# Kernel tuning notes

Hardware: AMD Instinct MI355X
Metric: run time of the kernel (lower is better)

Reference implementation:

```python
import jax, jax.numpy as jnp
import numpy as np

KH = KW = 3  # deform conv kernel
EPS = 1e-12  # F.normalize eps


def _deform_sample(img, u, v):
    """Flow-guided deformable sampling: bilinear gather of img at each of the
    9 kernel offsets shifted by the per-pixel flow (u=dx, v=dy).
    img: [B,C,H,W]; u,v: [B,1,H,W] -> returns [B,C,9,H,W]."""
    B, C, H, W = img.shape
    ky, kx = jnp.meshgrid(jnp.arange(KH) - 1, jnp.arange(KW) - 1, indexing='ij')
    ky = ky.reshape(1, 9, 1, 1).astype(img.dtype)
    kx = kx.reshape(1, 9, 1, 1).astype(img.dtype)
    iy = jnp.arange(H, dtype=img.dtype).reshape(1, 1, H, 1)
    ix = jnp.arange(W, dtype=img.dtype).reshape(1, 1, 1, W)
    py = iy + ky + v  # [B,9,H,W]
    px = ix + kx + u
    y0 = jnp.floor(py); x0 = jnp.floor(px)
    wy = py - y0; wx = px - x0  # bilinear weights
    y0i = y0.astype(jnp.int32); x0i = x0.astype(jnp.int32)
    flat = img.reshape(B, C, H * W)

    def gather(yi, xi):
        valid = ((yi >= 0) & (yi < H) & (xi >= 0) & (xi < W)).astype(img.dtype)
        idx = jnp.clip(yi, 0, H - 1) * W + jnp.clip(xi, 0, W - 1)  # [B,9,H,W]
        g = jax.vmap(lambda f, i: jnp.take(f, i.reshape(-1), axis=1))(flat, idx)
        return g.reshape(B, C, 9, H, W) * valid[:, None]

    s = (gather(y0i, x0i) * ((1 - wy) * (1 - wx))[:, None]
         + gather(y0i, x0i + 1) * ((1 - wy) * wx)[:, None]
         + gather(y0i + 1, x0i) * (wy * (1 - wx))[:, None]
         + gather(y0i + 1, x0i + 1) * (wy * wx)[:, None])
    return s


def setup_inputs() -> dict:
    key = jax.random.key(0)
    k1, k2, k3, k4, k5 = jax.random.split(key, 5)
    B, C, H, W = 2, 64, 256, 256
    num_heads = 4
    clone = jax.random.normal(k1, (B, C, H, W), dtype=jnp.float32)
    x = jax.random.normal(k2, (B, C, H * W), dtype=jnp.float32)
    u = jax.random.normal(k3, (B, 1, H, W), dtype=jnp.float32)
    v = jax.random.normal(k4, (B, 1, H, W), dtype=jnp.float32)
    weight = jax.random.normal(k5, (C, C, KH, KW), dtype=jnp.float32) * 0.05
    temperature = jnp.ones((num_heads, 1, 1), dtype=jnp.float32)
    return {"clone": clone, "x": x, "u": u, "v": v,
            "weight": weight, "temperature": temperature}


def reference(clone, x, u, v, weight, temperature):
    # deformable conv: bilinear gather then contract over (in_ch, kernel)
    s = _deform_sample(clone, u, v)                      # [B,C,9,H,W]
    w = weight.reshape(weight.shape[0], weight.shape[1], 9)
    conv = jnp.einsum('bckhw,ock->bohw', s, w)           # [B,C,H,W]
    B, C, H, W = conv.shape
    head = temperature.shape[0]
    kv = conv.reshape(B, head, C // head, H * W)          # k = v = deform output
    q = x.reshape(B, head, C // head, H * W)
    qn = q / jnp.maximum(jnp.linalg.norm(q, axis=-1, keepdims=True), EPS)
    kn = kv / jnp.maximum(jnp.linalg.norm(kv, axis=-1, keepdims=True), EPS)
    attn = jnp.einsum('bhcs,bhds->bhcd', qn, kn) * temperature  # [B,h,c,c]
    attn = jax.nn.softmax(attn, axis=-1)
    out = jnp.einsum('bhcd,bhds->bhcs', attn, kv)
    return out.reshape(B, C, H * W)
```

## Files before the change

### kernel.cpp

```cpp
#include <hip/hip_runtime.h>

typedef __bf16 bf16;
typedef __bf16 bf16x4 __attribute__((ext_vector_type(4)));
typedef __bf16 bf16x8 __attribute__((ext_vector_type(8)));
typedef float  f32x4  __attribute__((ext_vector_type(4)));

#define HH 256
#define WW 256
#define NB 2
#define NC 64
#define NS 65536
#define EX 258
#define NHEAD 4
#define DH 16

#define OFF_CLONET 0ul
#define OFF_CEXT   16777216ul
#define OFF_KV     33817600ul
#define OFF_WPK    50594816ul
#define OFF_ACC    50668544ul

__global__ __launch_bounds__(256) void k0t(const float* __restrict__ clone,
                                           bf16* __restrict__ cloneT,
                                           const float* __restrict__ wgt,
                                           bf16* __restrict__ wpk,
                                           float* __restrict__ accums) {
    const int xc = blockIdx.x;
    const int y  = blockIdx.y;
    const int b  = blockIdx.z;
    const int t  = threadIdx.x;

    if (b == 0 && y < 7) {
        int t2 = (y * 4 + xc) * 256 + t;
        if (t2 < 9 * 2 * 4 * 64) {
            int L   = t2 & 63;
            int mtg = (t2 >> 6) & 3;
            int kc  = (t2 >> 8) & 1;
            int tap = t2 >> 9;
            int o  = mtg * 16 + (L & 15);
            int cb = kc * 32 + (L >> 4) * 8;
            bf16x8 vv;
            #pragma unroll
            for (int j = 0; j < 8; j++)
                vv[j] = (bf16)wgt[(o * 64 + (cb + j)) * 9 + tap];
            *(bf16x8*)(wpk + t2 * 8) = vv;
        }
        int z = t2 - 9 * 2 * 4 * 64;
        if (z >= 0 && z < 2304) accums[z] = 0.0f;
    }

    __shared__ bf16 sm[64 * 68];
    {
        const int c = t >> 2, q = t & 3;
        const float* src = clone + ((size_t)(b * NC + c) * HH + y) * WW + xc * 64 + q * 16;
        #pragma unroll
        for (int i = 0; i < 4; i++) {
            f32x4 f = *(const f32x4*)(src + i * 4);
            bf16x4 h;
            #pragma unroll
            for (int j = 0; j < 4; j++) h[j] = (bf16)f[j];
            *(bf16x4*)(sm + c * 68 + q * 16 + i * 4) = h;
        }
    }
    __syncthreads();
    {
        const int x = t >> 2, cq = t & 3;
        bf16x8 o0, o1;
        #pragma unroll
        for (int j = 0; j < 8; j++) {
            o0[j] = sm[(cq * 16 + j) * 68 + x];
            o1[j] = sm[(cq * 16 + 8 + j) * 68 + x];
        }
        bf16* dst = cloneT + (((size_t)(b * HH + y) * WW + xc * 64 + x) << 6) + cq * 16;
        *(bf16x8*)(dst)     = o0;
        *(bf16x8*)(dst + 8) = o1;
    }
}

__global__ __launch_bounds__(256, 2) void k1_conv(const bf16* __restrict__ cloneT,
                                                  const bf16* __restrict__ wpk,
                                                  bf16* __restrict__ cext) {
    const int Xt = blockIdx.x;
    const int Yt = blockIdx.y;
    const int b  = blockIdx.z;
    const int t  = threadIdx.x;
    const int L  = t & 63;
    const int wv = t >> 6;
    const int mpair = wv >> 1;
    const int npair = wv & 1;

    extern __shared__ bf16 tile[];

    bf16x8 afrag[2][9][2];
    #pragma unroll
    for (int mt = 0; mt < 2; mt++)
        #pragma unroll
        for (int tap = 0; tap < 9; tap++)
            #pragma unroll
            for (int kc = 0; kc < 2; kc++) {
                int idx = ((tap * 2 + kc) * 4 + (mpair * 2 + mt)) * 64 + L;
                afrag[mt][tap][kc] = *(const bf16x8*)(wpk + idx * 8);
            }

    for (int r = 0; r < 8; r++) {
        int y = Yt * 6 - 2 + r;
        bool yin = (y >= 0) && (y < HH);
        for (int j = t; j < 528; j += 256) {
            int col = j >> 3, ck = j & 7;
            int xg = Xt * 64 - 2 + col;
            bf16x8 val;
            if (yin && xg >= 0 && xg < WW) {
                val = *(const bf16x8*)(cloneT + (((size_t)(b * HH + y) * WW + xg) << 6) + ck * 8);
            } else {
                #pragma unroll
                for (int e = 0; e < 8; e++) val[e] = (bf16)0.0f;
            }
            *(bf16x8*)(tile + (r * 66 + col) * 72 + ck * 8) = val;
        }
    }
    __syncthreads();

    const f32x4 zero4 = {0.0f, 0.0f, 0.0f, 0.0f};
    for (int Yi = 0; Yi < 6; Yi++) {
        f32x4 acc[2][2];
        acc[0][0] = zero4; acc[0][1] = zero4; acc[1][0] = zero4; acc[1][1] = zero4;
        #pragma unroll
        for (int tap = 0; tap < 9; tap++) {
            const int ky = tap / 3 - 1;
            const int kx = tap % 3 - 1;
            const int r = Yi + 1 + ky;
            #pragma unroll
            for (int kc = 0; kc < 2; kc++) {
                const int cb = kc * 32 + (L >> 4) * 8;
                #pragma unroll
                for (int nt = 0; nt < 2; nt++) {
                    const int col = npair * 32 + nt * 16 + (L & 15) + kx + 1;
                    bf16x8 bfrag = *(const bf16x8*)(tile + (r * 66 + col) * 72 + cb);
                    #pragma unroll
                    for (int mt = 0; mt < 2; mt++)
                        acc[mt][nt] = __builtin_amdgcn_mfma_f32_16x16x32_bf16(
                            afrag[mt][tap][kc], bfrag, acc[mt][nt], 0, 0, 0);
                }
            }
        }
        int Yp = Yt * 6 + Yi;
        #pragma unroll
        for (int mt = 0; mt < 2; mt++)
            #pragma unroll
            for (int nt = 0; nt < 2; nt++) {
                int Xp = Xt * 64 + npair * 32 + nt * 16 + (L & 15);
                if (Xp < EX) {
                    int o = mpair * 32 + mt * 16 + (L >> 4) * 4;
                    bf16x4 st;
                    #pragma unroll
                    for (int rg = 0; rg < 4; rg++) st[rg] = (bf16)acc[mt][nt][rg];
                    *(bf16x4*)(cext + ((((size_t)b * EX + Yp) * EX + Xp) << 6) + o) = st;
                }
            }
    }
}

__global__ __launch_bounds__(256) void k2_gather(const float* __restrict__ uu,
                                                 const float* __restrict__ vv,
                                                 const bf16* __restrict__ cext,
                                                 bf16* __restrict__ kv) {
    int gid = blockIdx.x * 256 + threadIdx.x;
    int ckh = gid >> 17;
    int idx = gid & 131071;
    int b  = idx >> 16;
    int hw = idx & 65535;
    int hy = hw >> 8;
    int wx = hw & 255;
    float fv = vv[idx];
    float fu = uu[idx];
    float py = (float)hy + fv;
    float px = (float)wx + fu;
    float fy = floorf(py);
    float fx = floorf(px);
    float ay = py - fy;
    float ax = px - fx;
    int ys = (int)fy + 1;
    int xs = (int)fx + 1;
    float w00 = (1.0f - ay) * (1.0f - ax);
    float w01 = (1.0f - ay) * ax;
    float w10 = ay * (1.0f - ax);
    float w11 = ay * ax;
    bool y0i = (ys >= 0) && (ys < EX);
    bool y1i = (ys + 1 >= 0) && (ys + 1 < EX);
    bool x0i = (xs >= 0) && (xs < EX);
    bool x1i = (xs + 1 >= 0) && (xs + 1 < EX);
    if (!y0i) { w00 = 0.0f; w01 = 0.0f; }
    if (!y1i) { w10 = 0.0f; w11 = 0.0f; }
    if (!x0i) { w00 = 0.0f; w10 = 0.0f; }
    if (!x1i) { w01 = 0.0f; w11 = 0.0f; }
    int y0c = ys < 0 ? 0 : (ys > EX - 1 ? EX - 1 : ys);
    int y1c = ys + 1 < 0 ? 0 : (ys + 1 > EX - 1 ? EX - 1 : ys + 1);
    int x0c = xs < 0 ? 0 : (xs > EX - 1 ? EX - 1 : xs);
    int x1c = xs + 1 < 0 ? 0 : (xs + 1 > EX - 1 ? EX - 1 : xs + 1);
    const bf16* pb = cext + (((size_t)b * EX * EX) << 6);
    size_t i00 = ((size_t)(y0c * EX + x0c)) << 6;
    size_t i01 = ((size_t)(y0c * EX + x1c)) << 6;
    size_t i10 = ((size_t)(y1c * EX + x0c)) << 6;
    size_t i11 = ((size_t)(y1c * EX + x1c)) << 6;
    bf16* kvp = kv + (((size_t)(b * NC + ckh * 32)) << 16) + hw;
    #pragma unroll
    for (int ck = 0; ck < 4; ck++) {
        int c0 = ckh * 32 + ck * 8;
        bf16x8 c00 = *(const bf16x8*)(pb + i00 + c0);
        bf16x8 c01 = *(const bf16x8*)(pb + i01 + c0);
        bf16x8 c10 = *(const bf16x8*)(pb + i10 + c0);
        bf16x8 c11 = *(const bf16x8*)(pb + i11 + c0);
        #pragma unroll
        for (int j = 0; j < 8; j++) {
            float val = w00 * (float)c00[j] + w01 * (float)c01[j]
                      + w10 * (float)c10[j] + w11 * (float)c11[j];
            kvp[((size_t)(ck * 8 + j)) << 16] = (bf16)val;
        }
    }
}

__global__ __launch_bounds__(256) void k3_dots(const float* __restrict__ x,
                                               const bf16* __restrict__ kv,
                                               float* __restrict__ dots,
                                               float* __restrict__ qss,
                                               float* __restrict__ kss) {
    const int ch = blockIdx.x;
    const int h  = blockIdx.y;
    const int b  = blockIdx.z;
    const int t  = threadIdx.x;
    const int L  = t & 63;
    const int wv = t >> 6;
    const int row = L & 15;
    const int kg  = L >> 4;
    const float* qb = x + ((size_t)(b * NC + h * DH + row)) * NS;
    const bf16*  kb = kv + (((size_t)(b * NC + h * DH + row)) << 16);
    f32x4 acc = {0.0f, 0.0f, 0.0f, 0.0f};
    float qp = 0.0f, kp = 0.0f;
    const int s0 = ch * 1024 + wv * 256 + kg * 8;
    for (int it = 0; it < 8; it++) {
        int s = s0 + it * 32;
        f32x4 q0 = *(const f32x4*)(qb + s);
        f32x4 q1 = *(const f32x4*)(qb + s + 4);
        bf16x8 ka = *(const bf16x8*)(kb + s);
        bf16x8 qa;
        #pragma unroll
        for (int j = 0; j < 4; j++) {
            qa[j]     = (bf16)q0[j];
            qa[j + 4] = (bf16)q1[j];
        }
        qp += q0[0]*q0[0] + q0[1]*q0[1] + q0[2]*q0[2] + q0[3]*q0[3]
            + q1[0]*q1[0] + q1[1]*q1[1] + q1[2]*q1[2] + q1[3]*q1[3];
        #pragma unroll
        for (int j = 0; j < 8; j++) {
            float kf = (float)ka[j];
            kp += kf * kf;
        }
        acc = __builtin_amdgcn_mfma_f32_16x16x32_bf16(qa, ka, acc, 0, 0, 0);
    }
    __shared__ float ldsD[256];
    __shared__ float ldsQ[16];
    __shared__ float ldsK[16];
    ldsD[t] = 0.0f;
    if (t < 16) { ldsQ[t] = 0.0f; ldsK[t] = 0.0f; }
    __syncthreads();
    #pragma unroll
    for (int rg = 0; rg < 4; rg++)
        atomicAdd(&ldsD[(kg * 4 + rg) * 16 + row], acc[rg]);
    atomicAdd(&ldsQ[row], qp);
    atomicAdd(&ldsK[row], kp);
    __syncthreads();
    const int bh = b * NHEAD + h;
    atomicAdd(&dots[bh * 256 + t], ldsD[t]);
    if (t < 16) {
        atomicAdd(&qss[bh * 16 + t], ldsQ[t]);
        atomicAdd(&kss[bh * 16 + t], ldsK[t]);
    }
}

__global__ __launch_bounds__(256) void k5_out(const bf16* __restrict__ kv,
                                              const float* __restrict__ dots,
                                              const float* __restrict__ qss,
                                              const float* __restrict__ kss,
                                              const float* __restrict__ temp,
                                              float* __restrict__ out) {
    const int ci = blockIdx.x;
    const int h  = blockIdx.y;
    const int b  = blockIdx.z;
    const int t  = threadIdx.x;
    const int bh = b * NHEAD + h;
    __shared__ float l[256];
    __shared__ float a[256];
    {
        int i = t >> 4, j = t & 15;
        float qn = fmaxf(sqrtf(qss[bh * 16 + i]), 1e-12f);
        float kn = fmaxf(sqrtf(kss[bh * 16 + j]), 1e-12f);
        float logit = dots[bh * 256 + t] / (qn * kn) * temp[h];
        l[t] = logit;
        __syncthreads();
        float mx = -1e30f;
        #pragma unroll
        for (int jj = 0; jj < 16; jj++) mx = fmaxf(mx, l[i * 16 + jj]);
        float sum = 0.0f;
        #pragma unroll
        for (int jj = 0; jj < 16; jj++) sum += expf(l[i * 16 + jj] - mx);
        a[t] = expf(logit - mx) / sum;
        __syncthreads();
    }
    const int s = (ci * 256 + t) * 4;
    const bf16* kvb = kv + (((size_t)(b * NC + h * DH)) << 16) + s;
    f32x4 kf[16];
    #pragma unroll
    for (int j = 0; j < 16; j++) {
        bf16x4 kk = *(const bf16x4*)(kvb + ((size_t)j << 16));
        #pragma unroll
        for (int e = 0; e < 4; e++) kf[j][e] = (float)kk[e];
    }
    float* ob = out + ((size_t)(b * NC + h * DH)) * NS + s;
    #pragma unroll
    for (int i = 0; i < 16; i++) {
        f32x4 o = {0.0f, 0.0f, 0.0f, 0.0f};
        #pragma unroll
        for (int j = 0; j < 16; j++)
            o += a[i * 16 + j] * kf[j];
        *(f32x4*)(ob + (size_t)i * NS) = o;
    }
}

extern "C" void kernel_launch(void* const* d_in, const int* in_sizes, int n_in,
                              void* d_out, int out_size, void* d_ws, size_t ws_size,
                              hipStream_t stream) {
    const float* clone = (const float*)d_in[0];
    const float* x     = (const float*)d_in[1];
    const float* u     = (const float*)d_in[2];
    const float* v     = (const float*)d_in[3];
    const float* wgt   = (const float*)d_in[4];
    const float* temp  = (const float*)d_in[5];
    float* out = (float*)d_out;

    char* ws = (char*)d_ws;
    bf16*  cloneT = (bf16*) (ws + OFF_CLONET);
    bf16*  cext   = (bf16*) (ws + OFF_CEXT);
    bf16*  kv     = (bf16*) (ws + OFF_KV);
    bf16*  wpk    = (bf16*) (ws + OFF_WPK);
    float* accums = (float*)(ws + OFF_ACC);
    float* dots = accums;
    float* qss  = accums + 2048;
    float* kss  = accums + 2048 + 128;

    static bool attr_set = false;
    if (!attr_set) {
        hipFuncSetAttribute((const void*)k1_conv,
                            hipFuncAttributeMaxDynamicSharedMemorySize, 76032);
        attr_set = true;
    }

    k0t<<<dim3(4, 256, 2), 256, 0, stream>>>(clone, cloneT, wgt, wpk, accums);
    k1_conv<<<dim3(5, 43, 2), 256, 76032, stream>>>(cloneT, wpk, cext);
    k2_gather<<<1024, 256, 0, stream>>>(u, v, cext, kv);
    k3_dots<<<dim3(64, 4, 2), 256, 0, stream>>>(x, kv, dots, qss, kss);
    k5_out<<<dim3(64, 4, 2), 256, 0, stream>>>(kv, dots, qss, kss, temp, out);
}
```

Baseline: 184.7 us.

## Fuse clone transpose into conv tile load and merge gather with dots

Removes the separate transpose kernel. The conv kernel now reads fp32 clone directly, converting and transposing it into its LDS tile, which drops one full bf16 intermediate write and read. It also fuses the bilinear gather kernel with the q·k dot-product kernel, so each block gathers 256 pixels of kv and then reduces dots for all four heads on those pixels. The cost is a wider LDS tile, strided fp32 loads in the conv prologue, and global atomics from more blocks per head. The dots phase re-reads the kv values the same block just wrote, after a block barrier.

```diff
diff --git a/kernel.cpp b/kernel.cpp
--- a/kernel.cpp
+++ b/kernel.cpp
@@ -14,70 +14,32 @@
 #define NHEAD 4
 #define DH 16
 
-#define OFF_CLONET 0ul
-#define OFF_CEXT   16777216ul
-#define OFF_KV     33817600ul
-#define OFF_WPK    50594816ul
-#define OFF_ACC    50668544ul
-
-__global__ __launch_bounds__(256) void k0t(const float* __restrict__ clone,
-                                           bf16* __restrict__ cloneT,
-                                           const float* __restrict__ wgt,
-                                           bf16* __restrict__ wpk,
-                                           float* __restrict__ accums) {
-    const int xc = blockIdx.x;
-    const int y  = blockIdx.y;
-    const int b  = blockIdx.z;
-    const int t  = threadIdx.x;
-
-    if (b == 0 && y < 7) {
-        int t2 = (y * 4 + xc) * 256 + t;
-        if (t2 < 9 * 2 * 4 * 64) {
-            int L   = t2 & 63;
-            int mtg = (t2 >> 6) & 3;
-            int kc  = (t2 >> 8) & 1;
-            int tap = t2 >> 9;
-            int o  = mtg * 16 + (L & 15);
-            int cb = kc * 32 + (L >> 4) * 8;
-            bf16x8 vv;
-            #pragma unroll
-            for (int j = 0; j < 8; j++)
-                vv[j] = (bf16)wgt[(o * 64 + (cb + j)) * 9 + tap];
-            *(bf16x8*)(wpk + t2 * 8) = vv;
-        }
-        int z = t2 - 9 * 2 * 4 * 64;
-        if (z >= 0 && z < 2304) accums[z] = 0.0f;
-    }
-
-    __shared__ bf16 sm[64 * 68];
-    {
-        const int c = t >> 2, q = t & 3;
-        const float* src = clone + ((size_t)(b * NC + c) * HH + y) * WW + xc * 64 + q * 16;
-        #pragma unroll
-        for (int i = 0; i < 4; i++) {
-            f32x4 f = *(const f32x4*)(src + i * 4);
-            bf16x4 h;
-            #pragma unroll
-            for (int j = 0; j < 4; j++) h[j] = (bf16)f[j];
-            *(bf16x4*)(sm + c * 68 + q * 16 + i * 4) = h;
-        }
-    }
-    __syncthreads();
-    {
-        const int x = t >> 2, cq = t & 3;
-        bf16x8 o0, o1;
-        #pragma unroll
-        for (int j = 0; j < 8; j++) {
-            o0[j] = sm[(cq * 16 + j) * 68 + x];
-            o1[j] = sm[(cq * 16 + 8 + j) * 68 + x];
-        }
-        bf16* dst = cloneT + (((size_t)(b * HH + y) * WW + xc * 64 + x) << 6) + cq * 16;
-        *(bf16x8*)(dst)     = o0;
-        *(bf16x8*)(dst + 8) = o1;
-    }
-}
-
-__global__ __launch_bounds__(256, 2) void k1_conv(const bf16* __restrict__ cloneT,
+#define OFF_CEXT   0ul
+#define OFF_KV     17040384ul
+#define OFF_WPK    33817600ul
+#define OFF_ACC    33891328ul
+
+__global__ void k0w(const float* __restrict__ wgt, bf16* __restrict__ wpk,
+                    float* __restrict__ accums) {
+    int t = blockIdx.x * 256 + threadIdx.x;
+    if (t < 9 * 2 * 4 * 64) {
+        int L   = t & 63;
+        int mtg = (t >> 6) & 3;
+        int kc  = (t >> 8) & 1;
+        int tap = t >> 9;
+        int o  = mtg * 16 + (L & 15);
+        int cb = kc * 32 + (L >> 4) * 8;
+        bf16x8 vv;
+        #pragma unroll
+        for (int j = 0; j < 8; j++)
+            vv[j] = (bf16)wgt[(o * 64 + (cb + j)) * 9 + tap];
+        *(bf16x8*)(wpk + t * 8) = vv;
+    }
+    int z = t - 9 * 2 * 4 * 64;
+    if (z >= 0 && z < 2304) accums[z] = 0.0f;
+}
+
+__global__ __launch_bounds__(256, 2) void k1_conv(const float* __restrict__ clone,
                                                   const bf16* __restrict__ wpk,
                                                   bf16* __restrict__ cext) {
     const int Xt = blockIdx.x;
@@ -102,20 +64,36 @@
                 afrag[mt][tap][kc] = *(const bf16x8*)(wpk + idx * 8);
             }
 
-    for (int r = 0; r < 8; r++) {
-        int y = Yt * 6 - 2 + r;
+    for (int u = t; u < 2176; u += 256) {
+        int xq = u % 17;
+        int rc = u / 17;
+        int cg = rc & 15;
+        int r  = rc >> 4;
+        int y  = Yt * 6 - 2 + r;
+        int xg0 = Xt * 64 - 4 + xq * 4;
+        int c0 = cg * 4;
+        f32x4 f[4];
         bool yin = (y >= 0) && (y < HH);
-        for (int j = t; j < 528; j += 256) {
-            int col = j >> 3, ck = j & 7;
-            int xg = Xt * 64 - 2 + col;
-            bf16x8 val;
-            if (yin && xg >= 0 && xg < WW) {
-                val = *(const bf16x8*)(cloneT + (((size_t)(b * HH + y) * WW + xg) << 6) + ck * 8);
-            } else {
+        if (yin && xg0 >= 0 && xg0 + 3 < WW) {
+            #pragma unroll
+            for (int i = 0; i < 4; i++)
+                f[i] = *(const f32x4*)(clone + ((size_t)(b * NC + c0 + i) * HH + y) * WW + xg0);
+        } else {
+            #pragma unroll
+            for (int i = 0; i < 4; i++)
                 #pragma unroll
-                for (int e = 0; e < 8; e++) val[e] = (bf16)0.0f;
-            }
-            *(bf16x8*)(tile + (r * 66 + col) * 72 + ck * 8) = val;
+                for (int e = 0; e < 4; e++) {
+                    int xg = xg0 + e;
+                    f[i][e] = (yin && xg >= 0 && xg < WW)
+                            ? clone[((size_t)(b * NC + c0 + i) * HH + y) * WW + xg] : 0.0f;
+                }
+        }
+        #pragma unroll
+        for (int e = 0; e < 4; e++) {
+            bf16x4 h;
+            #pragma unroll
+            for (int i = 0; i < 4; i++) h[i] = (bf16)f[i][e];
+            *(bf16x4*)(tile + (r * 68 + xq * 4 + e) * 72 + c0) = h;
         }
     }
     __syncthreads();
@@ -134,8 +112,8 @@
                 const int cb = kc * 32 + (L >> 4) * 8;
                 #pragma unroll
                 for (int nt = 0; nt < 2; nt++) {
-                    const int col = npair * 32 + nt * 16 + (L & 15) + kx + 1;
-                    bf16x8 bfrag = *(const bf16x8*)(tile + (r * 66 + col) * 72 + cb);
+                    const int col = npair * 32 + nt * 16 + (L & 15) + kx + 3;
+                    bf16x8 bfrag = *(const bf16x8*)(tile + (r * 68 + col) * 72 + cb);
                     #pragma unroll
                     for (int mt = 0; mt < 2; mt++)
                         acc[mt][nt] = __builtin_amdgcn_mfma_f32_16x16x32_bf16(
@@ -160,85 +138,88 @@
     }
 }
 
-__global__ __launch_bounds__(256) void k2_gather(const float* __restrict__ uu,
-                                                 const float* __restrict__ vv,
-                                                 const bf16* __restrict__ cext,
-                                                 bf16* __restrict__ kv) {
-    int gid = blockIdx.x * 256 + threadIdx.x;
-    int ckh = gid >> 17;
-    int idx = gid & 131071;
-    int b  = idx >> 16;
-    int hw = idx & 65535;
-    int hy = hw >> 8;
-    int wx = hw & 255;
-    float fv = vv[idx];
-    float fu = uu[idx];
-    float py = (float)hy + fv;
-    float px = (float)wx + fu;
-    float fy = floorf(py);
-    float fx = floorf(px);
-    float ay = py - fy;
-    float ax = px - fx;
-    int ys = (int)fy + 1;
-    int xs = (int)fx + 1;
-    float w00 = (1.0f - ay) * (1.0f - ax);
-    float w01 = (1.0f - ay) * ax;
-    float w10 = ay * (1.0f - ax);
-    float w11 = ay * ax;
-    bool y0i = (ys >= 0) && (ys < EX);
-    bool y1i = (ys + 1 >= 0) && (ys + 1 < EX);
-    bool x0i = (xs >= 0) && (xs < EX);
-    bool x1i = (xs + 1 >= 0) && (xs + 1 < EX);
-    if (!y0i) { w00 = 0.0f; w01 = 0.0f; }
-    if (!y1i) { w10 = 0.0f; w11 = 0.0f; }
-    if (!x0i) { w00 = 0.0f; w10 = 0.0f; }
-    if (!x1i) { w01 = 0.0f; w11 = 0.0f; }
-    int y0c = ys < 0 ? 0 : (ys > EX - 1 ? EX - 1 : ys);
-    int y1c = ys + 1 < 0 ? 0 : (ys + 1 > EX - 1 ? EX - 1 : ys + 1);
-    int x0c = xs < 0 ? 0 : (xs > EX - 1 ? EX - 1 : xs);
-    int x1c = xs + 1 < 0 ? 0 : (xs + 1 > EX - 1 ? EX - 1 : xs + 1);
-    const bf16* pb = cext + (((size_t)b * EX * EX) << 6);
-    size_t i00 = ((size_t)(y0c * EX + x0c)) << 6;
-    size_t i01 = ((size_t)(y0c * EX + x1c)) << 6;
-    size_t i10 = ((size_t)(y1c * EX + x0c)) << 6;
-    size_t i11 = ((size_t)(y1c * EX + x1c)) << 6;
-    bf16* kvp = kv + (((size_t)(b * NC + ckh * 32)) << 16) + hw;
-    #pragma unroll
-    for (int ck = 0; ck < 4; ck++) {
-        int c0 = ckh * 32 + ck * 8;
-        bf16x8 c00 = *(const bf16x8*)(pb + i00 + c0);
-        bf16x8 c01 = *(const bf16x8*)(pb + i01 + c0);
-        bf16x8 c10 = *(const bf16x8*)(pb + i10 + c0);
-        bf16x8 c11 = *(const bf16x8*)(pb + i11 + c0);
-        #pragma unroll
-        for (int j = 0; j < 8; j++) {
-            float val = w00 * (float)c00[j] + w01 * (float)c01[j]
-                      + w10 * (float)c10[j] + w11 * (float)c11[j];
-            kvp[((size_t)(ck * 8 + j)) << 16] = (bf16)val;
-        }
-    }
-}
-
-__global__ __launch_bounds__(256) void k3_dots(const float* __restrict__ x,
-                                               const bf16* __restrict__ kv,
-                                               float* __restrict__ dots,
-                                               float* __restrict__ qss,
-                                               float* __restrict__ kss) {
-    const int ch = blockIdx.x;
-    const int h  = blockIdx.y;
-    const int b  = blockIdx.z;
+
+__global__ __launch_bounds__(256) void k23(const float* __restrict__ uu,
+                                           const float* __restrict__ vv,
+                                           const bf16* __restrict__ cext,
+                                           const float* __restrict__ x,
+                                           bf16* __restrict__ kv,
+                                           float* __restrict__ dots,
+                                           float* __restrict__ qss,
+                                           float* __restrict__ kss) {
+    const int ci = blockIdx.x;
+    const int b  = blockIdx.y;
     const int t  = threadIdx.x;
-    const int L  = t & 63;
-    const int wv = t >> 6;
+
+    #pragma unroll
+    for (int it2 = 0; it2 < 2; it2++) {
+        int unit = it2 * 256 + t;
+        int ckh = unit >> 8;
+        int pix = unit & 255;
+        int hw = ci * 256 + pix;
+        int idx = b * NS + hw;
+        int hy = hw >> 8;
+        int wx = hw & 255;
+        float fv = vv[idx];
+        float fu = uu[idx];
+        float py = (float)hy + fv;
+        float px = (float)wx + fu;
+        float fy = floorf(py);
+        float fx = floorf(px);
+        float ay = py - fy;
+        float ax = px - fx;
+        int ys = (int)fy + 1;
+        int xs = (int)fx + 1;
+        float w00 = (1.0f - ay) * (1.0f - ax);
+        float w01 = (1.0f - ay) * ax;
+        float w10 = ay * (1.0f - ax);
+        float w11 = ay * ax;
+        bool y0i = (ys >= 0) && (ys < EX);
+        bool y1i = (ys + 1 >= 0) && (ys + 1 < EX);
+        bool x0i = (xs >= 0) && (xs < EX);
+        bool x1i = (xs + 1 >= 0) && (xs + 1 < EX);
+        if (!y0i) { w00 = 0.0f; w01 = 0.0f; }
+        if (!y1i) { w10 = 0.0f; w11 = 0.0f; }
+        if (!x0i) { w00 = 0.0f; w10 = 0.0f; }
+        if (!x1i) { w01 = 0.0f; w11 = 0.0f; }
+        int y0c = ys < 0 ? 0 : (ys > EX - 1 ? EX - 1 : ys);
+        int y1c = ys + 1 < 0 ? 0 : (ys + 1 > EX - 1 ? EX - 1 : ys + 1);
+        int x0c = xs < 0 ? 0 : (xs > EX - 1 ? EX - 1 : xs);
+        int x1c = xs + 1 < 0 ? 0 : (xs + 1 > EX - 1 ? EX - 1 : xs + 1);
+        const bf16* pb = cext + (((size_t)b * EX * EX) << 6);
+        size_t i00 = ((size_t)(y0c * EX + x0c)) << 6;
+        size_t i01 = ((size_t)(y0c * EX + x1c)) << 6;
+        size_t i10 = ((size_t)(y1c * EX + x0c)) << 6;
+        size_t i11 = ((size_t)(y1c * EX + x1c)) << 6;
+        bf16* kvp = kv + (((size_t)(b * NC + ckh * 32)) << 16) + hw;
+        #pragma unroll
+        for (int ck = 0; ck < 4; ck++) {
+            int c0 = ckh * 32 + ck * 8;
+            bf16x8 c00 = *(const bf16x8*)(pb + i00 + c0);
+            bf16x8 c01 = *(const bf16x8*)(pb + i01 + c0);
+            bf16x8 c10 = *(const bf16x8*)(pb + i10 + c0);
+            bf16x8 c11 = *(const bf16x8*)(pb + i11 + c0);
+            #pragma unroll
+            for (int j = 0; j < 8; j++) {
+                float val = w00 * (float)c00[j] + w01 * (float)c01[j]
+                          + w10 * (float)c10[j] + w11 * (float)c11[j];
+                kvp[((size_t)(ck * 8 + j)) << 16] = (bf16)val;
+            }
+        }
+    }
+    __syncthreads();
+
+    const int L = t & 63;
+    const int w = t >> 6;
     const int row = L & 15;
     const int kg  = L >> 4;
-    const float* qb = x + ((size_t)(b * NC + h * DH + row)) * NS;
-    const bf16*  kb = kv + (((size_t)(b * NC + h * DH + row)) << 16);
+    const float* qb = x  + ((size_t)(b * NC + w * DH + row)) * NS;
+    const bf16*  kb = kv + (((size_t)(b * NC + w * DH + row)) << 16);
     f32x4 acc = {0.0f, 0.0f, 0.0f, 0.0f};
     float qp = 0.0f, kp = 0.0f;
-    const int s0 = ch * 1024 + wv * 256 + kg * 8;
-    for (int it = 0; it < 8; it++) {
-        int s = s0 + it * 32;
+    const int s0 = ci * 256 + kg * 8;
+    for (int iter = 0; iter < 8; iter++) {
+        int s = s0 + iter * 32;
         f32x4 q0 = *(const f32x4*)(qb + s);
         f32x4 q1 = *(const f32x4*)(qb + s + 4);
         bf16x8 ka = *(const bf16x8*)(kb + s);
@@ -257,23 +238,25 @@
         }
         acc = __builtin_amdgcn_mfma_f32_16x16x32_bf16(qa, ka, acc, 0, 0, 0);
     }
-    __shared__ float ldsD[256];
-    __shared__ float ldsQ[16];
-    __shared__ float ldsK[16];
-    ldsD[t] = 0.0f;
-    if (t < 16) { ldsQ[t] = 0.0f; ldsK[t] = 0.0f; }
+    __shared__ float ldsD[1024];
+    __shared__ float ldsQ[64];
+    __shared__ float ldsK[64];
+    #pragma unroll
+    for (int w2 = 0; w2 < 4; w2++) ldsD[w2 * 256 + t] = 0.0f;
+    if (t < 64) { ldsQ[t] = 0.0f; ldsK[t] = 0.0f; }
     __syncthreads();
     #pragma unroll
     for (int rg = 0; rg < 4; rg++)
-        atomicAdd(&ldsD[(kg * 4 + rg) * 16 + row], acc[rg]);
-    atomicAdd(&ldsQ[row], qp);
-    atomicAdd(&ldsK[row], kp);
+        atomicAdd(&ldsD[w * 256 + (kg * 4 + rg) * 16 + row], acc[rg]);
+    atomicAdd(&ldsQ[w * 16 + row], qp);
+    atomicAdd(&ldsK[w * 16 + row], kp);
     __syncthreads();
-    const int bh = b * NHEAD + h;
-    atomicAdd(&dots[bh * 256 + t], ldsD[t]);
-    if (t < 16) {
-        atomicAdd(&qss[bh * 16 + t], ldsQ[t]);
-        atomicAdd(&kss[bh * 16 + t], ldsK[t]);
+    #pragma unroll
+    for (int w2 = 0; w2 < 4; w2++)
+        atomicAdd(&dots[(b * NHEAD + w2) * 256 + t], ldsD[w2 * 256 + t]);
+    if (t < 64) {
+        atomicAdd(&qss[b * 64 + t], ldsQ[t]);
+        atomicAdd(&kss[b * 64 + t], ldsK[t]);
     }
 }
 
@@ -338,7 +321,6 @@
     float* out = (float*)d_out;
 
     char* ws = (char*)d_ws;
-    bf16*  cloneT = (bf16*) (ws + OFF_CLONET);
     bf16*  cext   = (bf16*) (ws + OFF_CEXT);
     bf16*  kv     = (bf16*) (ws + OFF_KV);
     bf16*  wpk    = (bf16*) (ws + OFF_WPK);
@@ -350,13 +332,12 @@
     static bool attr_set = false;
     if (!attr_set) {
         hipFuncSetAttribute((const void*)k1_conv,
-                            hipFuncAttributeMaxDynamicSharedMemorySize, 76032);
+                            hipFuncAttributeMaxDynamicSharedMemorySize, 78336);
         attr_set = true;
     }
 
-    k0t<<<dim3(4, 256, 2), 256, 0, stream>>>(clone, cloneT, wgt, wpk, accums);
-    k1_conv<<<dim3(5, 43, 2), 256, 76032, stream>>>(cloneT, wpk, cext);
-    k2_gather<<<1024, 256, 0, stream>>>(u, v, cext, kv);
-    k3_dots<<<dim3(64, 4, 2), 256, 0, stream>>>(x, kv, dots, qss, kss);
+    k0w<<<27, 256, 0, stream>>>(wgt, wpk, accums);
+    k1_conv<<<dim3(5, 43, 2), 256, 78336, stream>>>(clone, wpk, cext);
+    k23<<<dim3(256, 2), 256, 0, stream>>>(u, v, cext, x, kv, dots, qss, kss);
     k5_out<<<dim3(64, 4, 2), 256, 0, stream>>>(kv, dots, qss, kss, temp, out);
 }
```

After: 172.5 us. 6.6% less time.
